# Performance work log

Hardware: AMD Instinct MI355X
Metric: run time of the kernel (lower is better)

## Reference

```python
import jax, jax.numpy as jnp
import numpy as np
from jax import lax

# dims
B, N, K = 8, 1024, 32          # batch, nodes, kNN neighbors
D, H, DH = 256, 8, 32           # node feature width, heads, head dim
TDIM, NB, HID = 16, 32, 128     # time-embed dim, radial basis count, radial MLP hidden
NLAYERS = 3                     # hidden transformer layers
L = NLAYERS + 1                 # + output layer
NS = 128                        # scalar channels sliced into edge attrs
SHD = 9                         # spherical harmonics dim for lmax=2 (1+3+5)
RMAX = 2.0
EIN = NB + TDIM + 2 * NS        # edge-MLP input width


def _sph(u):
    # real spherical harmonics l=0,1,2 with 'component' normalization of unit vec u
    x, y, z = u[..., 0], u[..., 1], u[..., 2]
    l0 = jnp.ones_like(x)[..., None]
    l1 = np.sqrt(3.0) * u
    l2 = jnp.stack([
        np.sqrt(15.0) * x * y,
        np.sqrt(15.0) * y * z,
        0.5 * np.sqrt(5.0) * (3.0 * z * z - 1.0),
        np.sqrt(15.0) * x * z,
        0.5 * np.sqrt(15.0) * (x * x - y * y),
    ], -1)
    return jnp.concatenate([l0, l1, l2], -1)


def _rbf(r):
    # e3nn soft_one_hot_linspace(basis='gaussian', cutoff=False) * sqrt(NB) * 0.95
    centers = jnp.linspace(0.0, RMAX, NB)
    step = RMAX / (NB - 1)
    e = jnp.exp(-((r[..., None] - centers) / step) ** 2) / 1.12
    return e * (NB ** 0.5) * 0.95


def _sus(x):
    # e3nn smooth unit step: exp(-1/x) for x>0 else 0
    return jnp.where(x > 0, jnp.exp(-1.0 / jnp.where(x > 0, x, 1.0)), 0.0)


def setup_inputs() -> dict:
    key = jax.random.key(0)
    ks = jax.random.split(key, 12)
    g = lambda k, shape, fan: (jax.random.normal(k, shape, jnp.float32) / np.sqrt(fan))
    return {
        'x': jax.random.normal(ks[0], (B, N, 3), jnp.float32),
        'y': jax.random.normal(ks[1], (B, N, 3), jnp.float32),
        't': jax.random.uniform(ks[2], (B, TDIM), jnp.float32),
        'W_embed': g(ks[3], (3 + TDIM, D), 3 + TDIM),
        'Wk1': g(ks[4], (L, EIN, HID), EIN),
        'bk1': jnp.zeros((L, HID), jnp.float32),
        'Wk2': g(ks[5], (L, HID, H * DH), HID),
        'Wq': g(ks[6], (L, D, H * DH), D),
        'Wv': g(ks[7], (L, D + SHD, H * DH), D + SHD),
        'Wo': g(ks[8], (NLAYERS, H * DH, D), H * DH),
        'Wo_out': g(ks[9], (H * DH, 3), H * DH),
    }


def _forward(x, y, t, W_embed, Wk1, bk1, Wk2, Wq, Wv, Wo, Wo_out):
    def score(pos, feat, tt):
        # kNN graph: full pairwise distance + top_k (self included, as in source)
        d2 = jnp.sum((pos[:, None, :] - pos[None, :, :]) ** 2, -1)      # [N,N]
        src = lax.top_k(-d2, K)[1]                                       # [N,K], dst = row index
        vec = pos[:, None, :] - pos[src]                                 # pos[dst]-pos[src], [N,K,3]
        r = jnp.linalg.norm(vec, axis=-1)                                # [N,K]
        u = vec / jnp.maximum(r[..., None], 1e-9)
        sh = _sph(u)                                                     # [N,K,SHD]
        cut = 1.4 * _sus(10.0 * (1.0 - r / RMAX))                        # [N,K]
        rbf = _rbf(r) * cut[..., None]                                   # [N,K,NB]
        t_nodes = jnp.broadcast_to(tt, (N, TDIM))
        edge_base = jnp.concatenate([rbf, jnp.broadcast_to(tt, (N, K, TDIM))], -1)
        node = jnp.concatenate([feat, t_nodes], -1) @ W_embed            # [N,D]
        for l in range(L):
            # gather scalar node channels onto edges
            e = jnp.concatenate([edge_base, node[src][..., :NS],
                                 jnp.broadcast_to(node[:, None, :NS], (N, K, NS))], -1)  # [N,K,EIN]
            h = jax.nn.gelu(e @ Wk1[l] + bk1[l])                          # radial MLP
            kf = (h @ Wk2[l]).reshape(N, K, H, DH)
            q = (node @ Wq[l]).reshape(N, H, DH)
            logits = jnp.einsum('nhd,nkhd->nkh', q, kf) / np.sqrt(DH)
            # cutoff-weighted softmax over neighbors (e3nn Transformer style)
            w = cut[..., None] * jnp.exp(logits - logits.max(1, keepdims=True))
            alpha = w / (w.sum(1, keepdims=True) + 1e-9)                  # [N,K,H]
            v = (jnp.concatenate([node[src], sh], -1) @ Wv[l]).reshape(N, K, H, DH)
            agg = jnp.einsum('nkh,nkhd->nhd', alpha, v).reshape(N, H * DH)
            if l < NLAYERS:
                node = node + agg @ Wo[l]                                  # residual
                # scalar activation: gelu on 0e, tanh on 0o, identity on higher l
                node = jnp.concatenate([jax.nn.gelu(node[:, :64]),
                                        jnp.tanh(node[:, 64:NS]),
                                        node[:, NS:]], -1)
            else:
                node = agg @ Wo_out                                        # project to 1x1e
        return node  # [N,3]

    return jax.vmap(score)(x, y, t)


def reference(x, y, t, W_embed, Wk1, bk1, Wk2, Wq, Wv, Wo, Wo_out):
    return _forward(x, y, t, W_embed, Wk1, bk1, Wk2, Wq, Wv, Wo, Wo_out)
```

## Files before the change

kernel.cpp:

```cpp
#include <hip/hip_runtime.h>
#include <math.h>

#define Bb 8
#define Nn 1024
#define Kk 32
#define Dd 256
#define Hh 8
#define DHh 32
#define TDIMt 16
#define NBnb 32
#define HIDh 128
#define NSns 128
#define SHDs 9
#define EINe 304
#define NCOLS 1536

typedef __bf16 bf16_t;
typedef bf16_t bf16x8 __attribute__((ext_vector_type(8)));
typedef bf16_t bf16x4v __attribute__((ext_vector_type(4)));
typedef float floatx4 __attribute__((ext_vector_type(4)));

#define GLOAD_LDS16(gp, lp) __builtin_amdgcn_global_load_lds( \
    (const __attribute__((address_space(1))) void*)(gp),      \
    (__attribute__((address_space(3))) void*)(lp), 16, 0, 0)

__device__ __forceinline__ float gelu_fast(float x){
  float g = 1.5957691216057308f*(x + 0.044715f*x*x*x);
  return x*__builtin_amdgcn_rcpf(1.0f + __expf(-g));
}
__device__ __forceinline__ float tanh_fast(float x){
  return 1.0f - 2.0f*__builtin_amdgcn_rcpf(1.0f + __expf(2.0f*x));
}

__global__ __launch_bounds__(256) void setup_kernel(
    const float* __restrict__ x, const float* __restrict__ y, const float* __restrict__ t,
    const float* __restrict__ We, const float* __restrict__ Wk1, const float* __restrict__ bk1,
    const float* __restrict__ Wk2, const float* __restrict__ Wq, const float* __restrict__ Wv,
    const float* __restrict__ Wo,
    bf16_t* __restrict__ Wt, bf16_t* __restrict__ Wto, bf16_t* __restrict__ WrbfT,
    float* __restrict__ t_hd, int* __restrict__ src,
    float* __restrict__ node, bf16_t* __restrict__ node_bf){

  __shared__ float s_b[32];
  __shared__ unsigned long long s_knn[4][64];
  const int bid = blockIdx.x, tid = threadIdx.x;

  if (bid < 2048){
    int wave = tid >> 6, lane = tid & 63;
    int bn = bid*4 + wave;
    int b = bn >> 10, n = bn & (Nn-1);
    const float* xb = x + (size_t)b*Nn*3;
    float px = xb[n*3+0], py = xb[n*3+1], pz = xb[n*3+2];
    float d2v[16];
    #pragma unroll
    for (int i=0;i<16;i++){
      int j = i*64 + lane;
      float dx = px - xb[j*3+0];
      float dy = py - xb[j*3+1];
      float dz = pz - xb[j*3+2];
      d2v[i] = dx*dx + dy*dy + dz*dz;
    }

    unsigned lob = 0u, hib = 0x7149F2CAu;
    float T = 1.0f;
    int lc = 0;
    for (int it=0; it<24; ++it){
      lc = 0;
      #pragma unroll
      for (int i=0;i<16;i++) lc += (d2v[i] <= T) ? 1 : 0;
      int c = lc;
      #pragma unroll
      for (int off=32; off>=1; off>>=1) c += __shfl_xor(c, off);
      if (c >= 32 && c <= 64) break;
      if (c < 32) lob = __float_as_uint(T); else hib = __float_as_uint(T);
      float ratio = 44.0f * __builtin_amdgcn_rcpf((float)(c < 1 ? 1 : c));
      float Tn = T * __powf(ratio, 0.6666667f);
      unsigned tb = __float_as_uint(Tn);
      if (tb <= lob || tb >= hib) tb = lob + ((hib - lob) >> 1);
      T = __uint_as_float(tb);
    }

    int pre = lc;
    #pragma unroll
    for (int d=1; d<64; d<<=1){
      int o = __shfl_up(pre, d);
      if (lane >= d) pre += o;
    }
    int wo = pre - lc;

    unsigned long long* sl = s_knn[wave];
    sl[lane] = ~0ull;
    #pragma unroll
    for (int i=0;i<16;i++){
      if (d2v[i] <= T && wo < 64){
        sl[wo] = (((unsigned long long)__float_as_uint(d2v[i])) << 10)
                 | (unsigned)(i*64 + lane);
        wo++;
      }
    }
    __syncthreads();

    unsigned long long key = sl[lane];
    #pragma unroll
    for (int k2=2; k2<=64; k2<<=1){
      #pragma unroll
      for (int j2=k2>>1; j2>=1; j2>>=1){
        unsigned long long pv = __shfl_xor(key, j2);
        bool takeMin = (((lane & j2) == 0) == ((lane & k2) == 0));
        bool pLess = pv < key;
        key = (pLess == takeMin) ? pv : key;
      }
    }
    if (lane < 32) src[(size_t)bn*Kk + lane] = (int)(key & 1023u);
  } else if (bid < 6144){
    int i = bid-2048; int l = i>>10, yy = i&1023;
    int h = yy>>7, c = yy&127;
    if (tid < 32) s_b[tid] = Wk2[(size_t)l*HIDh*Dd + (size_t)c*Dd + h*DHh + tid];
    __syncthreads();
    const int rloc = tid>>3, dg = tid&7;
    const float b0 = s_b[dg*4+0], b1 = s_b[dg*4+1], b2 = s_b[dg*4+2], b3 = s_b[dg*4+3];
    #pragma unroll
    for (int p=0;p<8;p++){
      int ii = p*32 + rloc;
      const float4 v = *(const float4*)(Wq + (size_t)l*Dd*Dd + (size_t)ii*Dd + h*DHh + dg*4);
      float part = v.x*b0 + v.y*b1 + v.z*b2 + v.w*b3;
      part += __shfl_xor(part, 1);
      part += __shfl_xor(part, 2);
      part += __shfl_xor(part, 4);
      if (dg == 0) Wt[((size_t)l*NCOLS + 512 + yy)*Dd + ii] = (bf16_t)part;
    }
  } else if (bid < 8192){
    int i = bid-6144; int l = i>>9, c = i&511, k = tid;
    const float* wk1l = Wk1 + (size_t)l*EINe*HIDh;
    float v;
    if (c < 256)       v = Wv[(size_t)l*265*Dd + (size_t)k*Dd + c];
    else if (c < 384){ int c2 = c-256; v = (k < 128) ? wk1l[(48+k)*HIDh + c2] : 0.0f; }
    else             { int c2 = c-384; v = (k < 128) ? wk1l[(176+k)*HIDh + c2] : 0.0f; }
    Wt[((size_t)l*NCOLS + c)*Dd + k] = (bf16_t)v;
  } else if (bid < 8960){
    int i = bid-8192; int l = i>>8; int c = i&255; int k = tid;
    Wto[((size_t)l*Dd + c)*Dd + k] = (bf16_t)Wo[(size_t)l*Dd*Dd + (size_t)k*Dd + c];
  } else if (bid < 9024){
    int i = bid-8960; int l = i>>4, cg = i&15;
    int c = cg*8 + (tid>>5), k = tid&31;
    WrbfT[((size_t)l*HIDh + c)*NBnb + k] = (bf16_t)Wk1[(size_t)l*EINe*HIDh + (size_t)k*HIDh + c];
  } else if (bid < 9040){
    int i = bid-9024; int pair = i*2 + (tid>>7);
    int l = pair>>3, b = pair&7, c = tid&127;
    const float* wk1l = Wk1 + (size_t)l*EINe*HIDh;
    float a = bk1[l*HIDh + c];
    #pragma unroll
    for (int ii=0;ii<TDIMt;ii++) a += t[b*TDIMt+ii]*wk1l[(32+ii)*HIDh + c];
    t_hd[(l*Bb + b)*HIDh + c] = a;
  } else {
    int bn0 = (bid-9040)*4; int c = tid;
    float w0 = We[0*Dd+c], w1 = We[1*Dd+c], w2 = We[2*Dd+c];
    float wt[TDIMt];
    #pragma unroll
    for (int i=0;i<TDIMt;i++) wt[i] = We[(3+i)*Dd+c];
    #pragma unroll
    for (int u=0;u<4;u++){
      int bn = bn0 + u; int b = bn >> 10;
      float a = y[(size_t)bn*3+0]*w0 + y[(size_t)bn*3+1]*w1 + y[(size_t)bn*3+2]*w2;
      #pragma unroll
      for (int i=0;i<TDIMt;i++) a += t[b*TDIMt+i]*wt[i];
      node[(size_t)bn*Dd + c] = a;
      node_bf[(size_t)bn*Dd + c] = (bf16_t)a;
    }
  }
}

__global__ __launch_bounds__(256) void gemm_proj(const bf16_t* __restrict__ A,
    const bf16_t* __restrict__ Wt_all, float* __restrict__ vproj_f,
    bf16_t* __restrict__ hsrc_bf, float* __restrict__ hdst_f,
    bf16_t* __restrict__ qw_bf, const float* __restrict__ t_hd, int layer){

  __shared__ __align__(16) bf16_t s_A[2][8192];
  __shared__ __align__(16) bf16_t s_B[2][4096];

  const int tid = threadIdx.x;
  const int wave = tid>>6, lane = tid&63;
  const int row16 = lane&15, quad = lane>>4;
  const int bx = blockIdx.x;
  const int brow = ((bx & 7) << 3) + (bx >> 3);
  const int m0 = brow*128;
  const int m_base = m0 + wave*32;
  const int n_base = blockIdx.y*64;
  const bf16_t* Ab = A + (size_t)m0*Dd;
  const bf16_t* Bw = Wt_all + ((size_t)layer*NCOLS + n_base)*Dd;

  const int trow = tid>>3;
  const int tk   = ((tid&7) ^ (trow&7)) << 3;
  const int swz  = (row16&7) << 3;

  floatx4 acc[2][4];
  #pragma unroll
  for (int mi=0;mi<2;mi++)
    #pragma unroll
    for (int ni=0;ni<4;ni++){ floatx4 z = {0.f,0.f,0.f,0.f}; acc[mi][ni] = z; }

  {
    const bf16_t* ga = Ab + (size_t)trow*Dd + tk;
    #pragma unroll
    for (int i=0;i<4;i++) GLOAD_LDS16(ga + (size_t)i*32*Dd, &s_A[0][i*2048 + tid*8]);
    const bf16_t* gb = Bw + (size_t)trow*Dd + tk;
    #pragma unroll
    for (int j=0;j<2;j++) GLOAD_LDS16(gb + (size_t)j*32*Dd, &s_B[0][j*2048 + tid*8]);
  }
  __syncthreads();

  #pragma unroll
  for (int kt=0; kt<4; kt++){
    const int cur = kt&1, nxt = cur^1;
    if (kt < 3){
      const bf16_t* ga = Ab + (size_t)trow*Dd + (kt+1)*64 + tk;
      #pragma unroll
      for (int i=0;i<4;i++) GLOAD_LDS16(ga + (size_t)i*32*Dd, &s_A[nxt][i*2048 + tid*8]);
      const bf16_t* gb = Bw + (size_t)trow*Dd + (kt+1)*64 + tk;
      #pragma unroll
      for (int j=0;j<2;j++) GLOAD_LDS16(gb + (size_t)j*32*Dd, &s_B[nxt][j*2048 + tid*8]);
    }
    #pragma unroll
    for (int ksub=0; ksub<2; ksub++){
      const int ko = (ksub*32 + quad*8) ^ swz;
      bf16x8 a0 = *(const bf16x8*)&s_A[cur][(wave*32      + row16)*64 + ko];
      bf16x8 a1 = *(const bf16x8*)&s_A[cur][(wave*32 + 16 + row16)*64 + ko];
      #pragma unroll
      for (int ni=0;ni<4;ni++){
        bf16x8 b = *(const bf16x8*)&s_B[cur][(ni*16 + row16)*64 + ko];
        acc[0][ni] = __builtin_amdgcn_mfma_f32_16x16x32_bf16(a0, b, acc[0][ni], 0,0,0);
        acc[1][ni] = __builtin_amdgcn_mfma_f32_16x16x32_bf16(a1, b, acc[1][ni], 0,0,0);
      }
    }
    __syncthreads();
  }

  const int by = blockIdx.y;
  const int bb = m_base >> 10;
  #pragma unroll
  for (int mi=0;mi<2;mi++)
    #pragma unroll
    for (int ni=0;ni<4;ni++){
      int col = n_base + ni*16 + row16;
      #pragma unroll
      for (int r=0;r<4;r++){
        int row = m_base + mi*16 + quad*4 + r;
        float v = acc[mi][ni][r];
        if (by < 4)       vproj_f[(size_t)row*256 + col]        = v;
        else if (by < 6)  hsrc_bf[(size_t)row*128 + (col-256)]  = (bf16_t)v;
        else if (by < 8)  hdst_f[(size_t)row*128 + (col-384)]   = v + t_hd[(size_t)(layer*Bb + bb)*HIDh + (col-384)];
        else              qw_bf[(size_t)row*1024 + (col-512)]   = (bf16_t)v;
      }
    }
}

__global__ __launch_bounds__(256) void gemm_upd(
    const bf16_t* __restrict__ agg_bf, const bf16_t* __restrict__ Wto,
    const float* __restrict__ node_in, float* __restrict__ node_out,
    bf16_t* __restrict__ node_bf, int lu, int write_node){

  __shared__ __align__(16) bf16_t s_A[2][8192];
  __shared__ __align__(16) bf16_t s_B[2][4096];

  const int tid = threadIdx.x;
  const int wave = tid>>6, lane = tid&63;
  const int row16 = lane&15, quad = lane>>4;
  const int bx = blockIdx.x;
  const int brow = ((bx & 7) << 3) + (bx >> 3);
  const int m0 = brow*128;
  const int m_base = m0 + wave*32;
  const int n_base = blockIdx.y*64;
  const bf16_t* Ab = agg_bf + (size_t)m0*Dd;
  const bf16_t* Bw = Wto + (size_t)lu*Dd*Dd + (size_t)n_base*Dd;

  const int trow = tid>>3;
  const int tk   = ((tid&7) ^ (trow&7)) << 3;
  const int swz  = (row16&7) << 3;

  floatx4 acc[2][4];
  #pragma unroll
  for (int mi=0;mi<2;mi++)
    #pragma unroll
    for (int ni=0;ni<4;ni++){ floatx4 z = {0.f,0.f,0.f,0.f}; acc[mi][ni] = z; }

  {
    const bf16_t* ga = Ab + (size_t)trow*Dd + tk;
    #pragma unroll
    for (int i=0;i<4;i++) GLOAD_LDS16(ga + (size_t)i*32*Dd, &s_A[0][i*2048 + tid*8]);
    const bf16_t* gb = Bw + (size_t)trow*Dd + tk;
    #pragma unroll
    for (int j=0;j<2;j++) GLOAD_LDS16(gb + (size_t)j*32*Dd, &s_B[0][j*2048 + tid*8]);
  }
  __syncthreads();

  #pragma unroll
  for (int kt=0; kt<4; kt++){
    const int cur = kt&1, nxt = cur^1;
    if (kt < 3){
      const bf16_t* ga = Ab + (size_t)trow*Dd + (kt+1)*64 + tk;
      #pragma unroll
      for (int i=0;i<4;i++) GLOAD_LDS16(ga + (size_t)i*32*Dd, &s_A[nxt][i*2048 + tid*8]);
      const bf16_t* gb = Bw + (size_t)trow*Dd + (kt+1)*64 + tk;
      #pragma unroll
      for (int j=0;j<2;j++) GLOAD_LDS16(gb + (size_t)j*32*Dd, &s_B[nxt][j*2048 + tid*8]);
    }
    #pragma unroll
    for (int ksub=0; ksub<2; ksub++){
      const int ko = (ksub*32 + quad*8) ^ swz;
      bf16x8 a0 = *(const bf16x8*)&s_A[cur][(wave*32      + row16)*64 + ko];
      bf16x8 a1 = *(const bf16x8*)&s_A[cur][(wave*32 + 16 + row16)*64 + ko];
      #pragma unroll
      for (int ni=0;ni<4;ni++){
        bf16x8 b = *(const bf16x8*)&s_B[cur][(ni*16 + row16)*64 + ko];
        acc[0][ni] = __builtin_amdgcn_mfma_f32_16x16x32_bf16(a0, b, acc[0][ni], 0,0,0);
        acc[1][ni] = __builtin_amdgcn_mfma_f32_16x16x32_bf16(a1, b, acc[1][ni], 0,0,0);
      }
    }
    __syncthreads();
  }

  #pragma unroll
  for (int mi=0;mi<2;mi++)
    #pragma unroll
    for (int ni=0;ni<4;ni++){
      int col = n_base + ni*16 + row16;
      #pragma unroll
      for (int r=0;r<4;r++){
        int row = m_base + mi*16 + quad*4 + r;
        float v = acc[mi][ni][r] + node_in[(size_t)row*Dd + col];
        if (col < 64)       v = gelu_fast(v);
        else if (col < 128) v = tanh_fast(v);
        if (write_node) node_out[(size_t)row*Dd + col] = v;
        node_bf[(size_t)row*Dd + col] = (bf16_t)v;
      }
    }
}

__global__ __launch_bounds__(256) void attn_kernel(
    const float* __restrict__ x, const int* __restrict__ src,
    const float* __restrict__ vproj_f, const bf16_t* __restrict__ hsrc_bf,
    const float* __restrict__ hdst_f, const bf16_t* __restrict__ qw_bf,
    const bf16_t* __restrict__ WrbfT,
    const float* __restrict__ Wvg, const float* __restrict__ Woo,
    bf16_t* __restrict__ agg_bf, float* __restrict__ out, int layer){

  __shared__ __align__(16) char smem[46080];
  const int tid  = threadIdx.x;
  const int wave = tid>>6, lane = tid&63;
  char* sw = smem + wave*11520;
  bf16_t* s_h   = (bf16_t*)(sw);
  float*  s_al  = (float*)(sw + 8704);
  float*  s_sh  = (float*)(sw + 9728);
  float*  s_cut = (float*)(sw + 11008);
  float*  s_pool= (float*)(sw + 11136);

  const int bidx = blockIdx.x;
  const int b    = bidx & 7;
  const int bn   = (b << 10) | ((bidx >> 3) << 2) | wave;
  const int row16 = lane&15, quad = lane>>4;

  bf16x8 qf[4];
  { const bf16_t* qp = qw_bf + (size_t)bn*1024 + row16*HIDh + quad*8;
    #pragma unroll
    for (int ks=0; ks<4; ks++) qf[ks] = *(const bf16x8*)(qp + ks*32); }
  float hdv[8];
  #pragma unroll
  for (int j=0; j<8; j++) hdv[j] = hdst_f[(size_t)bn*128 + j*16 + row16];

  const float ax = x[(size_t)bn*3+0], ay = x[(size_t)bn*3+1], az = x[(size_t)bn*3+2];

  bf16x8 hsv[8];
  {
    const int eg = lane>>1, half = lane&1;
    const int sG = src[(size_t)bn*Kk + eg];
    const bf16_t* hp = hsrc_bf + ((size_t)b*Nn + sG)*128 + half*64;
    #pragma unroll
    for (int j=0;j<8;j++) hsv[j] = *(const bf16x8*)(hp + j*8);
  }

  const int sE0 = src[(size_t)bn*Kk + row16];
  const int sE1 = src[(size_t)bn*Kk + row16 + 16];
  bf16x8 a0f, a1f;
  {
    const float* xj0 = x + ((size_t)b*Nn + sE0)*3;
    const float* xj1 = x + ((size_t)b*Nn + sE1)*3;
    float d0x = ax - xj0[0], d0y = ay - xj0[1], d0z = az - xj0[2];
    float d1x = ax - xj1[0], d1y = ay - xj1[1], d1z = az - xj1[2];
    float rr0 = sqrtf(d0x*d0x + d0y*d0y + d0z*d0z);
    float rr1 = sqrtf(d1x*d1x + d1y*d1y + d1z*d1z);
    float xx0 = 10.0f*(1.0f - rr0*0.5f);
    float xx1 = 10.0f*(1.0f - rr1*0.5f);
    float cu0 = (xx0 > 0.0f) ? 1.4f*__expf(-__builtin_amdgcn_rcpf(xx0)) : 0.0f;
    float cu1 = (xx1 > 0.0f) ? 1.4f*__expf(-__builtin_amdgcn_rcpf(xx1)) : 0.0f;
    float sc0 = 4.798224586623f*cu0;
    float sc1 = 4.798224586623f*cu1;
    float rs0 = fminf(rr0*15.5f, 33.0f);
    float rs1 = fminf(rr1*15.5f, 33.0f);
    float cbase = (float)(quad*8);
    float dd0 = rs0 - cbase, dd1 = rs1 - cbase;
    float e0v = __expf(-dd0*dd0)*sc0;
    float e1v = __expf(-dd1*dd1)*sc1;
    float g0 = __expf(2.0f*dd0 - 1.0f);
    float g1 = __expf(2.0f*dd1 - 1.0f);
    a0f[0] = (bf16_t)e0v; a1f[0] = (bf16_t)e1v;
    #pragma unroll
    for (int j=1;j<8;j++){
      e0v *= g0; e1v *= g1;
      a0f[j] = (bf16_t)e0v; a1f[j] = (bf16_t)e1v;
      g0 *= 0.13533528323661270f; g1 *= 0.13533528323661270f;
    }
  }

  {
    const int k = lane & 31;
    const int j = src[(size_t)bn*Kk + k];
    const float* xj = x + ((size_t)b*Nn + j)*3;
    float dx = ax - xj[0], dy = ay - xj[1], dz = az - xj[2];
    float rr = sqrtf(dx*dx + dy*dy + dz*dz);
    if (lane < 32){
      float xx = 10.0f*(1.0f - rr*0.5f);
      s_cut[k] = (xx > 0.0f) ? 1.4f*__expf(-__builtin_amdgcn_rcpf(xx)) : 0.0f;
    } else {
      float inv = __builtin_amdgcn_rcpf(fmaxf(rr, 1e-9f));
      float ux = dx*inv, uy = dy*inv, uz = dz*inv;
      float* sh = s_sh + k*10;
      sh[0] = 1.0f;
      sh[1] = 1.7320508075688772f*ux;
      sh[2] = 1.7320508075688772f*uy;
      sh[3] = 1.7320508075688772f*uz;
      sh[4] = 3.872983346207417f*ux*uy;
      sh[5] = 3.872983346207417f*uy*uz;
      sh[6] = 1.118033988749895f*(3.0f*uz*uz - 1.0f);
      sh[7] = 3.872983346207417f*ux*uz;
      sh[8] = 1.9364916731037085f*(ux*ux - uy*uy);
    }
  }

  floatx4 acc0[8], acc1[8];
  {
    const bf16_t* bp = WrbfT + ((size_t)layer*HIDh + row16)*NBnb + quad*8;
    #pragma unroll
    for (int j=0;j<8;j++){
      floatx4 z = {0.f,0.f,0.f,0.f};
      bf16x8 bbf = *(const bf16x8*)(bp + (size_t)j*16*NBnb);
      acc0[j] = __builtin_amdgcn_mfma_f32_16x16x32_bf16(a0f, bbf, z, 0,0,0);
      acc1[j] = __builtin_amdgcn_mfma_f32_16x16x32_bf16(a1f, bbf, z, 0,0,0);
    }
  }

  {
    const int eg = lane>>1, half = lane&1;
    #pragma unroll
    for (int j=0;j<8;j++)
      *(bf16x8*)(s_h + eg*136 + half*64 + j*8) = hsv[j];
  }

  #pragma unroll
  for (int j=0;j<8;j++){
    const int c = j*16 + row16;
    const float hd = hdv[j];
    #pragma unroll
    for (int r=0;r<4;r++){
      int e = quad*4 + r;
      float hs = (float)s_h[e*136 + c];
      s_h[e*136 + c] = (bf16_t)gelu_fast(acc0[j][r] + hd + hs);
    }
    #pragma unroll
    for (int r=0;r<4;r++){
      int e = 16 + quad*4 + r;
      float hs = (float)s_h[e*136 + c];
      s_h[e*136 + c] = (bf16_t)gelu_fast(acc1[j][r] + hd + hs);
    }
  }

  floatx4 la[2];
  #pragma unroll
  for (int rg=0; rg<2; rg++){
    floatx4 l4 = {0.f,0.f,0.f,0.f};
    #pragma unroll
    for (int ks=0; ks<4; ks++){
      bf16x8 a = *(const bf16x8*)(s_h + (rg*16 + row16)*136 + ks*32 + quad*8);
      l4 = __builtin_amdgcn_mfma_f32_16x16x32_bf16(a, qf[ks], l4, 0,0,0);
    }
    la[rg] = l4;
  }

  {
    float lv[8], ct[8];
    #pragma unroll
    for (int rg=0; rg<2; rg++)
      #pragma unroll
      for (int r=0;r<4;r++){
        lv[rg*4+r] = la[rg][r]*0.17677669529663687f;
        ct[rg*4+r] = s_cut[rg*16 + quad*4 + r];
      }
    float m = lv[0];
    #pragma unroll
    for (int i=1;i<8;i++) m = fmaxf(m, lv[i]);
    m = fmaxf(m, __shfl_xor(m, 16));
    m = fmaxf(m, __shfl_xor(m, 32));
    float w[8]; float ss = 0.f;
    #pragma unroll
    for (int i=0;i<8;i++){ w[i] = ct[i]*__expf(lv[i]-m); ss += w[i]; }
    ss += __shfl_xor(ss, 16);
    ss += __shfl_xor(ss, 32);
    float rs = __builtin_amdgcn_rcpf(ss + 1e-9f);
    if (row16 < Hh){
      #pragma unroll
      for (int rg=0; rg<2; rg++)
        #pragma unroll
        for (int r=0;r<4;r++)
          s_al[(rg*16 + quad*4 + r)*8 + row16] = w[rg*4+r]*rs;
    }
  }

  {
    const int h2 = lane>>3, sg = lane&7;
    float a = 0.0f;
    #pragma unroll
    for (int k2=0;k2<Kk;k2++)
      a += s_al[k2*8 + h2] * s_sh[k2*10 + sg];
    s_pool[h2*10 + sg] = a;
    if (lane < 8){
      float a8 = 0.0f;
      #pragma unroll
      for (int k2=0;k2<Kk;k2++)
        a8 += s_al[k2*8 + lane] * s_sh[k2*10 + 8];
      s_pool[lane*10 + 8] = a8;
    }
  }

  float4 accv = {0.f,0.f,0.f,0.f};
  {
    const int h = lane>>3;
    #pragma unroll
    for (int g=0; g<4; g++){
      const float* rp[8];
      #pragma unroll
      for (int i=0;i<8;i++){
        int row = __builtin_amdgcn_readfirstlane(src[(size_t)bn*Kk + g*8 + i]);
        rp[i] = vproj_f + ((size_t)b*Nn + row)*256;
      }
      #pragma unroll
      for (int i=0;i<8;i++){
        const float4 v = *(const float4*)(rp[i] + (lane<<2));
        float al = s_al[(g*8+i)*8 + h];
        accv.x += al*v.x; accv.y += al*v.y; accv.z += al*v.z; accv.w += al*v.w;
      }
    }
  }

  {
    const int h = lane>>3;
    const float* wvsh = Wvg + (size_t)layer*265*Dd + 256*Dd;
    #pragma unroll
    for (int sg=0; sg<SHDs; sg++){
      const float4 wv4 = *(const float4*)(wvsh + sg*Dd + (lane<<2));
      const float pl = s_pool[h*10 + sg];
      accv.x += pl*wv4.x; accv.y += pl*wv4.y; accv.z += pl*wv4.z; accv.w += pl*wv4.w;
    }

    if (layer < 3){
      bf16x4v o;
      o[0] = (bf16_t)accv.x; o[1] = (bf16_t)accv.y;
      o[2] = (bf16_t)accv.z; o[3] = (bf16_t)accv.w;
      *(bf16x4v*)(agg_bf + (size_t)bn*Dd + (lane<<2)) = o;
    } else {
      const int c0 = lane<<2;
      float p0 = accv.x*Woo[c0*3+0] + accv.y*Woo[c0*3+3] + accv.z*Woo[c0*3+6] + accv.w*Woo[c0*3+9];
      float p1 = accv.x*Woo[c0*3+1] + accv.y*Woo[c0*3+4] + accv.z*Woo[c0*3+7] + accv.w*Woo[c0*3+10];
      float p2 = accv.x*Woo[c0*3+2] + accv.y*Woo[c0*3+5] + accv.z*Woo[c0*3+8] + accv.w*Woo[c0*3+11];
      #pragma unroll
      for (int off=32; off>=1; off>>=1){
        p0 += __shfl_xor(p0, off);
        p1 += __shfl_xor(p1, off);
        p2 += __shfl_xor(p2, off);
      }
      if (lane == 0){
        out[(size_t)bn*3+0] = p0;
        out[(size_t)bn*3+1] = p1;
        out[(size_t)bn*3+2] = p2;
      }
    }
  }
}

extern "C" void kernel_launch(void* const* d_in, const int* in_sizes, int n_in,
                              void* d_out, int out_size, void* d_ws, size_t ws_size,
                              hipStream_t stream){
  const float* x   = (const float*)d_in[0];
  const float* y   = (const float*)d_in[1];
  const float* t   = (const float*)d_in[2];
  const float* We  = (const float*)d_in[3];
  const float* Wk1 = (const float*)d_in[4];
  const float* bk1 = (const float*)d_in[5];
  const float* Wk2 = (const float*)d_in[6];
  const float* Wq  = (const float*)d_in[7];
  const float* Wv  = (const float*)d_in[8];
  const float* Wo  = (const float*)d_in[9];
  const float* Woo = (const float*)d_in[10];
  float* out = (float*)d_out;

  char* ws = (char*)d_ws;
  size_t off = 0;
  auto take = [&](size_t bytes)->char*{ char* p = ws + off; off = (off + bytes + 255) & ~(size_t)255; return p; };

  int*    src      = (int*)   take((size_t)Bb*Nn*Kk*4);
  float*  nodeA    = (float*) take((size_t)Bb*Nn*Dd*4);
  float*  nodeB    = (float*) take((size_t)Bb*Nn*Dd*4);
  bf16_t* node_bf  = (bf16_t*)take((size_t)Bb*Nn*Dd*2);
  bf16_t* agg_bf   = (bf16_t*)take((size_t)Bb*Nn*Dd*2);
  float*  vproj_f  = (float*) take((size_t)Bb*Nn*256*4);
  bf16_t* hsrc_bf  = (bf16_t*)take((size_t)Bb*Nn*128*2);
  float*  hdst_f   = (float*) take((size_t)Bb*Nn*128*4);
  bf16_t* qw_bf    = (bf16_t*)take(((size_t)Bb*Nn*1024 + 2048)*2);
  bf16_t* Wt       = (bf16_t*)take((size_t)4*NCOLS*Dd*2);
  bf16_t* Wto      = (bf16_t*)take((size_t)3*Dd*Dd*2);
  bf16_t* WrbfT    = (bf16_t*)take((size_t)4*HIDh*NBnb*2);
  float*  t_hd     = (float*) take((size_t)4*Bb*HIDh*4);

  setup_kernel<<<dim3(11088), 256, 0, stream>>>(x, y, t, We, Wk1, bk1, Wk2, Wq, Wv, Wo,
                                                Wt, Wto, WrbfT, t_hd, src, nodeA, node_bf);

  gemm_proj<<<dim3(64,24), 256, 0, stream>>>(node_bf, Wt, vproj_f, hsrc_bf, hdst_f, qw_bf, t_hd, 0);
  attn_kernel<<<dim3(Bb*Nn/4), 256, 0, stream>>>(x, src, vproj_f, hsrc_bf, hdst_f, qw_bf,
                                                 WrbfT, Wv, Woo, agg_bf, out, 0);
  const float* nin[3]  = {nodeA, nodeB, nodeA};
  float*       nout[3] = {nodeB, nodeA, nodeB};
  for (int l=1; l<4; l++){
    gemm_upd<<<dim3(64,4), 256, 0, stream>>>(agg_bf, Wto, nin[l-1], nout[l-1], node_bf,
                                             l-1, (l < 3) ? 1 : 0);
    gemm_proj<<<dim3(64,24), 256, 0, stream>>>(node_bf, Wt, vproj_f, hsrc_bf, hdst_f, qw_bf, t_hd, l);
    attn_kernel<<<dim3(Bb*Nn/4), 256, 0, stream>>>(x, src, vproj_f, hsrc_bf, hdst_f, qw_bf,
                                                   WrbfT, Wv, Woo, agg_bf, out, l);
  }
}
```

Before: 383.6 us.

## Cut attention kernel register and LDS pressure to raise occupancy

The attention kernel now requests four blocks per CU through launch bounds. It shrinks per-wave shared memory by aliasing the alpha and pool buffers onto the s_h region once s_h is dead. Gathered source features are written straight into shared memory instead of being held in 8 vector registers. The radial MFMA and GELU stage is split into two halves to halve live accumulators, and a scheduling barrier is added. The risk is that the aliasing is only correct if s_h is not read after s_al and s_pool are written, and the gather-to-LDS store now sits earlier, which could serialize latency.

Result: faster. 370.3 us (-3.5%).

```diff
diff --git a/kernel.cpp b/kernel.cpp
--- a/kernel.cpp
+++ b/kernel.cpp
@@ -336,7 +336,7 @@
     }
 }
 
-__global__ __launch_bounds__(256) void attn_kernel(
+__global__ __launch_bounds__(256, 4) void attn_kernel(
     const float* __restrict__ x, const int* __restrict__ src,
     const float* __restrict__ vproj_f, const bf16_t* __restrict__ hsrc_bf,
     const float* __restrict__ hdst_f, const bf16_t* __restrict__ qw_bf,
@@ -344,15 +344,15 @@
     const float* __restrict__ Wvg, const float* __restrict__ Woo,
     bf16_t* __restrict__ agg_bf, float* __restrict__ out, int layer){
 
-  __shared__ __align__(16) char smem[46080];
+  __shared__ __align__(16) char smem[40448];
   const int tid  = threadIdx.x;
   const int wave = tid>>6, lane = tid&63;
-  char* sw = smem + wave*11520;
+  char* sw = smem + wave*10112;
   bf16_t* s_h   = (bf16_t*)(sw);
-  float*  s_al  = (float*)(sw + 8704);
-  float*  s_sh  = (float*)(sw + 9728);
-  float*  s_cut = (float*)(sw + 11008);
-  float*  s_pool= (float*)(sw + 11136);
+  float*  s_sh  = (float*)(sw + 8704);
+  float*  s_cut = (float*)(sw + 9984);
+  float*  s_al  = (float*)(sw);
+  float*  s_pool= (float*)(sw + 1024);
 
   const int bidx = blockIdx.x;
   const int b    = bidx & 7;
@@ -369,13 +369,13 @@
 
   const float ax = x[(size_t)bn*3+0], ay = x[(size_t)bn*3+1], az = x[(size_t)bn*3+2];
 
-  bf16x8 hsv[8];
   {
     const int eg = lane>>1, half = lane&1;
     const int sG = src[(size_t)bn*Kk + eg];
     const bf16_t* hp = hsrc_bf + ((size_t)b*Nn + sG)*128 + half*64;
     #pragma unroll
-    for (int j=0;j<8;j++) hsv[j] = *(const bf16x8*)(hp + j*8);
+    for (int j=0;j<8;j++)
+      *(bf16x8*)(s_h + eg*136 + half*64 + j*8) = *(const bf16x8*)(hp + j*8);
   }
 
   const int sE0 = src[(size_t)bn*Kk + row16];
@@ -436,40 +436,33 @@
     }
   }
 
-  floatx4 acc0[8], acc1[8];
-  {
+  #pragma unroll
+  for (int p=0; p<2; p++){
+    floatx4 acc0[4], acc1[4];
     const bf16_t* bp = WrbfT + ((size_t)layer*HIDh + row16)*NBnb + quad*8;
     #pragma unroll
-    for (int j=0;j<8;j++){
+    for (int j2=0;j2<4;j2++){
       floatx4 z = {0.f,0.f,0.f,0.f};
-      bf16x8 bbf = *(const bf16x8*)(bp + (size_t)j*16*NBnb);
-      acc0[j] = __builtin_amdgcn_mfma_f32_16x16x32_bf16(a0f, bbf, z, 0,0,0);
-      acc1[j] = __builtin_amdgcn_mfma_f32_16x16x32_bf16(a1f, bbf, z, 0,0,0);
-    }
-  }
-
-  {
-    const int eg = lane>>1, half = lane&1;
-    #pragma unroll
-    for (int j=0;j<8;j++)
-      *(bf16x8*)(s_h + eg*136 + half*64 + j*8) = hsv[j];
-  }
-
-  #pragma unroll
-  for (int j=0;j<8;j++){
-    const int c = j*16 + row16;
-    const float hd = hdv[j];
-    #pragma unroll
-    for (int r=0;r<4;r++){
-      int e = quad*4 + r;
-      float hs = (float)s_h[e*136 + c];
-      s_h[e*136 + c] = (bf16_t)gelu_fast(acc0[j][r] + hd + hs);
-    }
-    #pragma unroll
-    for (int r=0;r<4;r++){
-      int e = 16 + quad*4 + r;
-      float hs = (float)s_h[e*136 + c];
-      s_h[e*136 + c] = (bf16_t)gelu_fast(acc1[j][r] + hd + hs);
+      bf16x8 bbf = *(const bf16x8*)(bp + (size_t)(p*4+j2)*16*NBnb);
+      acc0[j2] = __builtin_amdgcn_mfma_f32_16x16x32_bf16(a0f, bbf, z, 0,0,0);
+      acc1[j2] = __builtin_amdgcn_mfma_f32_16x16x32_bf16(a1f, bbf, z, 0,0,0);
+    }
+    #pragma unroll
+    for (int j2=0;j2<4;j2++){
+      const int c = (p*4+j2)*16 + row16;
+      const float hd = hdv[p*4+j2];
+      #pragma unroll
+      for (int r=0;r<4;r++){
+        int e = quad*4 + r;
+        float hs = (float)s_h[e*136 + c];
+        s_h[e*136 + c] = (bf16_t)gelu_fast(acc0[j2][r] + hd + hs);
+      }
+      #pragma unroll
+      for (int r=0;r<4;r++){
+        int e = 16 + quad*4 + r;
+        float hs = (float)s_h[e*136 + c];
+        s_h[e*136 + c] = (bf16_t)gelu_fast(acc1[j2][r] + hd + hs);
+      }
     }
   }
 
@@ -484,6 +477,8 @@
     }
     la[rg] = l4;
   }
+
+  __builtin_amdgcn_sched_barrier(0);
 
   {
     float lv[8], ct[8];
```
